# Performance work log

Hardware: AMD Instinct MI355X
Metric: run time of the kernel (lower is better)

The kernel has to match this reference:

```python
import jax, jax.numpy as jnp
import numpy as np

EPS = 1e-5
H = 1024      # hidden_size
HH = 256      # hyper_hidden_size
E = 32        # hyper_embed_size
D = 512       # input_size
B = 4096      # batch
FORGET_BIAS = 1.0


def _ln(x, w, b):
    mu = x.mean(-1, keepdims=True)
    var = x.var(-1, keepdims=True)
    return (x - mu) * jax.lax.rsqrt(var + EPS) * w + b


def _chunk_ln(x, w, b, chunks):
    # normalize each of `chunks` equal slices independently, then single affine
    bsz = x.shape[0]
    u = x.shape[1] // chunks
    xr = x.reshape(bsz, chunks, u)
    mu = xr.mean(-1, keepdims=True)
    var = xr.var(-1, keepdims=True)
    xr = (xr - mu) * jax.lax.rsqrt(var + EPS)
    return xr.reshape(bsz, chunks * u) * w + b


def _ln_lstm_step(x, h, c, w_ih, w_hh, lnh_w, lnh_b, lnc_w, lnc_b):
    # LayerNormLSTMCell (dropout = identity, eval mode)
    lin = _chunk_ln(x @ w_ih.T + h @ w_hh.T, lnh_w, lnh_b, 4)
    i_g, f_g, o_g, c_cand = jnp.split(lin, 4, axis=1)
    c = jax.nn.sigmoid(f_g + FORGET_BIAS) * c + jax.nn.sigmoid(i_g) * jnp.tanh(c_cand)
    h = jax.nn.sigmoid(o_g) * jnp.tanh(_ln(c, lnc_w, lnc_b))
    return h, c


def _forward(x, h_total, c_total,
             hyp_w_ih, hyp_w_hh, hyp_lnh_w, hyp_lnh_b, hyp_lnc_w, hyp_lnc_b,
             w_ih, w_hh, lnh_w, lnh_b, lnc_w, lnc_b,
             sx_w0, sx_b0, sx_w1, sh_w0, sh_b0, sh_w1, bh_w0, bh_w1):
    h, h_hyper = h_total[:, :H], h_total[:, H:]
    c, c_hyper = c_total[:, :H], c_total[:, H:]

    h_hyper, c_hyper = _ln_lstm_step(x, h_hyper, c_hyper, hyp_w_ih, hyp_w_hh,
                                     hyp_lnh_w, hyp_lnh_b, hyp_lnc_w, hyp_lnc_b)

    bsz = x.shape[0]
    Wx = (x @ w_ih.T).reshape(bsz, 4, H)   # [B,4,H]
    Wh = (h @ w_hh.T).reshape(bsz, 4, H)

    # hypernetwork scale/bias nets, batched over the 4 gates (g)
    scale_x = jnp.einsum('bge,goe->bgo', jnp.einsum('bi,gei->bge', h_hyper, sx_w0) + sx_b0, sx_w1)
    scale_h = jnp.einsum('bge,goe->bgo', jnp.einsum('bi,gei->bge', h_hyper, sh_w0) + sh_b0, sh_w1)
    bias_h = jnp.einsum('bge,goe->bgo', jnp.einsum('bi,gei->bge', h_hyper, bh_w0), bh_w1)

    gates = (scale_x * Wx + scale_h * Wh + bias_h).reshape(bsz, 4 * H)
    gates = _chunk_ln(gates, lnh_w, lnh_b, 4)
    i_g, f_g, o_g, c_cand = jnp.split(gates, 4, axis=1)
    c = jax.nn.sigmoid(f_g + FORGET_BIAS) * c + jax.nn.sigmoid(i_g) * jnp.tanh(c_cand)
    h = jax.nn.sigmoid(o_g) * jnp.tanh(_ln(c, lnc_w, lnc_b))

    h_total = jnp.concatenate([h, h_hyper], axis=1)
    c_total = jnp.concatenate([c, c_hyper], axis=1)
    return h, h_total, c_total


def setup_inputs() -> dict:
    key = jax.random.key(0)
    ks = jax.random.split(key, 24)
    rn = lambda k, shape, s: jax.random.normal(k, shape, dtype=jnp.float32) * s
    inp = {
        'x': rn(ks[0], (B, D), 1.0),
        'h_total': rn(ks[1], (B, H + HH), 1.0),
        'c_total': rn(ks[2], (B, H + HH), 1.0),
        # hyper cell (LayerNormLSTMCell) params
        'hyp_w_ih': rn(ks[3], (4 * HH, D), 0.05),
        'hyp_w_hh': rn(ks[4], (4 * HH, HH), 0.06),
        'hyp_lnh_w': jnp.ones((4 * HH,), jnp.float32),
        'hyp_lnh_b': jnp.zeros((4 * HH,), jnp.float32),
        'hyp_lnc_w': jnp.ones((HH,), jnp.float32),
        'hyp_lnc_b': jnp.zeros((HH,), jnp.float32),
        # main cell params
        'w_ih': rn(ks[5], (4 * H, D), 0.04),
        'w_hh': rn(ks[6], (4 * H, H), 0.03),
        'lnh_w': jnp.ones((4 * H,), jnp.float32),
        'lnh_b': jnp.zeros((4 * H,), jnp.float32),
        'lnc_w': jnp.ones((H,), jnp.float32),
        'lnc_b': jnp.zeros((H,), jnp.float32),
        # norms_x: 4 HyperNorms (scale net only): Linear(HH->E, bias) + Linear(E->H, no bias)
        'sx_w0': rn(ks[7], (4, E, HH), 0.01),
        'sx_b0': jnp.ones((4, E), jnp.float32),
        'sx_w1': rn(ks[8], (4, H, E), 0.1 / E),
        # norms_h: scale net + bias net
        'sh_w0': rn(ks[9], (4, E, HH), 0.01),
        'sh_b0': jnp.ones((4, E), jnp.float32),
        'sh_w1': rn(ks[10], (4, H, E), 0.1 / E),
        'bh_w0': rn(ks[11], (4, E, HH), 0.01),
        'bh_w1': rn(ks[12], (4, H, E), 0.01),
    }
    return inp


def reference(x, h_total, c_total,
              hyp_w_ih, hyp_w_hh, hyp_lnh_w, hyp_lnh_b, hyp_lnc_w, hyp_lnc_b,
              w_ih, w_hh, lnh_w, lnh_b, lnc_w, lnc_b,
              sx_w0, sx_b0, sx_w1, sh_w0, sh_b0, sh_w1, bh_w0, bh_w1):
    return _forward(x, h_total, c_total,
                    hyp_w_ih, hyp_w_hh, hyp_lnh_w, hyp_lnh_b, hyp_lnc_w, hyp_lnc_b,
                    w_ih, w_hh, lnh_w, lnh_b, lnc_w, lnc_b,
                    sx_w0, sx_b0, sx_w1, sh_w0, sh_b0, sh_w1, bh_w0, bh_w1)
```

## Files before the change

### kernel.cpp

```cpp
#include <hip/hip_runtime.h>
#include <math.h>

typedef unsigned short u16;
typedef unsigned int u32;
typedef unsigned long long u64;
typedef __attribute__((ext_vector_type(4))) float vf4;
typedef __attribute__((ext_vector_type(8))) _Float16 f16x8;

#define EPSV 1e-5f
#define BB 4096
#define LDT 1280

__device__ __forceinline__ float sigf(float x){
  float e = expf(-fabsf(x));
  float r = 1.f/(1.f+e);
  return x>=0.f ? r : 1.f-r;
}

__device__ __forceinline__ float wave_sum(float v){
  #pragma unroll
  for (int m=32;m>0;m>>=1) v += __shfl_xor(v, m);
  return v;
}

#define AS1 __attribute__((address_space(1)))
#define AS3 __attribute__((address_space(3)))
__device__ __forceinline__ void gload_lds16(const u16* g, u16* l){
  __builtin_amdgcn_global_load_lds((const AS1 void*)g, (AS3 void*)l, 16, 0, 0);
}

__global__ __launch_bounds__(64) void cvt_half(const float* __restrict__ in, int ld_in, int K,
                                               u16* __restrict__ out, int ld_out)
{
  int row = blockIdx.y;
  int c4 = (blockIdx.x*64 + threadIdx.x)*4;
  if (c4 >= K) return;
  float4 v = *(const float4*)(in + (size_t)row*ld_in + c4);
  float vv[4] = {v.x, v.y, v.z, v.w};
  u64 pk=0;
  #pragma unroll
  for (int j=0;j<4;j++){
    _Float16 h = (_Float16)vv[j];
    pk |= (u64)__builtin_bit_cast(u16, h) << (16*j);
  }
  *(u64*)(out + (size_t)row*ld_out + c4) = pk;
}

template<int P>
__device__ __forceinline__ void load_afrag(const u16* Ab, int wm, int lm, int kg, f16x8 af[2][2]){
  #pragma unroll
  for (int fl=0; fl<2; fl++)
    #pragma unroll
    for (int kk=0; kk<2; kk++){
      int row = wm*128 + (P*2+fl)*16 + lm;
      int sl = (kk*4+kg) ^ (row&7);
      af[fl][kk] = *(const f16x8*)(Ab + row*64 + sl*8);
    }
}

template<int P>
__device__ __forceinline__ void mfma_phase(vf4 acc[8][4], const f16x8 af[2][2], const f16x8 bf[4][2]){
  __builtin_amdgcn_s_setprio(1);
  #pragma unroll
  for (int fl=0; fl<2; fl++)
    #pragma unroll
    for (int j=0; j<4; j++)
      #pragma unroll
      for (int kk=0; kk<2; kk++)
        acc[P*2+fl][j] = __builtin_amdgcn_mfma_f32_16x16x32_f16(af[fl][kk], bf[j][kk], acc[P*2+fl][j], 0, 0, 0);
  __builtin_amdgcn_s_setprio(0);
}

__global__ __launch_bounds__(512, 2) void gemm256(
    const u16* __restrict__ A, int lda,
    const u16* __restrict__ B, int ldb,
    float* __restrict__ C, int ldc, int K)
{
  __shared__ u16 As[2][256*64];
  __shared__ u16 Bs[2][256*64];
  const int tid = threadIdx.x;
  const int lane = tid & 63;
  const int wid = tid >> 6;
  const int wm = wid >> 2, wn = wid & 3;
  const int m0 = blockIdx.y*256, n0 = blockIdx.x*256;
  const int kg = lane>>4, lm = lane&15;

  vf4 acc[8][4];
  #pragma unroll
  for (int i=0;i<8;i++)
    #pragma unroll
    for (int j=0;j<4;j++) acc[i][j] = (vf4){0.f,0.f,0.f,0.f};

  const u16* gA[4]; const u16* gB[4]; int ldsOff[4];
  #pragma unroll
  for (int q=0;q<4;q++){
    int c = q*512 + tid;
    int row = c>>3, slot = c&7;
    int scol = slot ^ (row&7);
    gA[q] = A + (size_t)(m0+row)*lda + scol*8;
    gB[q] = B + (size_t)(n0+row)*ldb + scol*8;
    ldsOff[q] = (q*512 + wid*64)*8;
  }

  const int NT = K>>6;
  #pragma unroll
  for (int q=0;q<4;q++) gload_lds16(gA[q], &As[0][ldsOff[q]]);
  #pragma unroll
  for (int q=0;q<4;q++) gload_lds16(gB[q], &Bs[0][ldsOff[q]]);
  asm volatile("s_waitcnt vmcnt(0)" ::: "memory");
  __builtin_amdgcn_s_barrier();

  f16x8 afA[2][2], afB[2][2], bfrag[4][2];

  for (int t=0; t<NT; ++t){
    const int cur = t&1, nxt = cur^1;
    const u16* Ab = As[cur];
    const u16* Bb = Bs[cur];

    load_afrag<0>(Ab, wm, lm, kg, afA);
    #pragma unroll
    for (int j=0;j<4;j++)
      #pragma unroll
      for (int kk=0;kk<2;kk++){
        int row = wn*64 + j*16 + lm;
        int sl = (kk*4+kg) ^ (row&7);
        bfrag[j][kk] = *(const f16x8*)(Bb + row*64 + sl*8);
      }
    load_afrag<1>(Ab, wm, lm, kg, afB);
    if (t+1 < NT){
      const int kb = (t+1)<<6;
      #pragma unroll
      for (int q=0;q<4;q++) gload_lds16(gA[q]+kb, &As[nxt][ldsOff[q]]);
      #pragma unroll
      for (int q=0;q<4;q++) gload_lds16(gB[q]+kb, &Bs[nxt][ldsOff[q]]);
    }
    __builtin_amdgcn_sched_barrier(0);
    __builtin_amdgcn_s_barrier();
    mfma_phase<0>(acc, afA, bfrag);
    __builtin_amdgcn_s_barrier();

    load_afrag<2>(Ab, wm, lm, kg, afA);
    __builtin_amdgcn_sched_barrier(0);
    __builtin_amdgcn_s_barrier();
    mfma_phase<1>(acc, afB, bfrag);
    __builtin_amdgcn_s_barrier();

    load_afrag<3>(Ab, wm, lm, kg, afB);
    __builtin_amdgcn_sched_barrier(0);
    __builtin_amdgcn_s_barrier();
    mfma_phase<2>(acc, afA, bfrag);
    __builtin_amdgcn_s_barrier();

    __builtin_amdgcn_sched_barrier(0);
    __builtin_amdgcn_s_barrier();
    mfma_phase<3>(acc, afB, bfrag);
    asm volatile("s_waitcnt vmcnt(0)" ::: "memory");
    __builtin_amdgcn_s_barrier();
  }

  #pragma unroll
  for (int f=0; f<8; f++){
    int rb = m0 + wm*128 + f*16 + kg*4;
    #pragma unroll
    for (int j=0; j<4; j++){
      int cc = n0 + wn*64 + j*16 + lm;
      #pragma unroll
      for (int r=0; r<4; r++)
        C[(size_t)(rb+r)*ldc + cc] = acc[f][j][r];
    }
  }
}

__global__ __launch_bounds__(256) void gemm_f16nt(
    const u16* __restrict__ A, int lda,
    const u16* __restrict__ B, int ldb,
    float* __restrict__ C, int ldc,
    int K, int accflag)
{
  __shared__ u16 As[128*32];
  __shared__ u16 Bs[128*32];
  const int tid = threadIdx.x;
  const int lane = tid & 63;
  const int w = tid >> 6;
  const int wr = w >> 1, wc = w & 1;
  const int m0 = blockIdx.y*128, n0 = blockIdx.x*128;

  vf4 acc[4][4];
  #pragma unroll
  for (int i=0;i<4;i++)
    #pragma unroll
    for (int j=0;j<4;j++) acc[i][j] = (vf4){0.f,0.f,0.f,0.f};

  const int c0i = w*128 + lane;
  const int c1i = c0i + 64;
  const int r0i = c0i>>2, s0i = (c0i&3) ^ ((r0i>>1)&3);
  const int r1i = c1i>>2, s1i = (c1i&3) ^ ((r1i>>1)&3);
  const u16* gA0 = A + (size_t)(m0+r0i)*lda + s0i*8;
  const u16* gA1 = A + (size_t)(m0+r1i)*lda + s1i*8;
  const u16* gB0 = B + (size_t)(n0+r0i)*ldb + s0i*8;
  const u16* gB1 = B + (size_t)(n0+r1i)*ldb + s1i*8;
  u16* lA0 = As + w*1024;
  u16* lA1 = As + w*1024 + 512;
  u16* lB0 = Bs + w*1024;
  u16* lB1 = Bs + w*1024 + 512;

  const int kg = lane>>4, lm = lane&15;

  for (int k0=0; k0<K; k0+=32){
    __syncthreads();
    gload_lds16(gA0 + k0, lA0);
    gload_lds16(gA1 + k0, lA1);
    gload_lds16(gB0 + k0, lB0);
    gload_lds16(gB1 + k0, lB1);
    __syncthreads();
    f16x8 af[4], bfr[4];
    #pragma unroll
    for (int i=0;i<4;i++){
      int ra = wr*64 + i*16 + lm;
      int sa = kg ^ ((ra>>1)&3);
      af[i] = *(const f16x8*)(As + ra*32 + sa*8);
      int rb = wc*64 + i*16 + lm;
      int sb = kg ^ ((rb>>1)&3);
      bfr[i] = *(const f16x8*)(Bs + rb*32 + sb*8);
    }
    #pragma unroll
    for (int i=0;i<4;i++)
      #pragma unroll
      for (int j=0;j<4;j++)
        acc[i][j] = __builtin_amdgcn_mfma_f32_16x16x32_f16(af[i], bfr[j], acc[i][j], 0, 0, 0);
  }

  const int lhi = lane>>4;
  #pragma unroll
  for (int i=0;i<4;i++){
    int rbase = m0 + wr*64 + i*16 + lhi*4;
    #pragma unroll
    for (int j=0;j<4;j++){
      int cc = n0 + wc*64 + j*16 + lm;
      #pragma unroll
      for (int r=0;r<4;r++){
        float v = acc[i][j][r];
        float* pC = C + (size_t)(rbase+r)*ldc + cc;
        if (accflag) v += *pC;
        *pC = v;
      }
    }
  }
}

__global__ __launch_bounds__(256) void hyper_cell(
    const float* __restrict__ lin, const float* __restrict__ c_in,
    const float* __restrict__ lnh_w, const float* __restrict__ lnh_b,
    const float* __restrict__ lnc_w, const float* __restrict__ lnc_b,
    float* __restrict__ ht_out, float* __restrict__ ct_out)
{
  int b=blockIdx.x, tid=threadIdx.x, lane=tid&63, w=tid>>6;
  __shared__ float ly[1024];
  __shared__ float red[4];
  float4 t = *(const float4*)(lin + (size_t)b*1024 + tid*4);
  float v[4]={t.x,t.y,t.z,t.w};
  float s = wave_sum(v[0]+v[1]+v[2]+v[3]);
  float mu = s*(1.f/256.f);
  float q=0.f;
  #pragma unroll
  for (int j=0;j<4;j++){ float d=v[j]-mu; q+=d*d; }
  q = wave_sum(q);
  float rs = rsqrtf(q*(1.f/256.f)+EPSV);
  int base = tid*4;
  #pragma unroll
  for (int j=0;j<4;j++) ly[base+j] = (v[j]-mu)*rs*lnh_w[base+j]+lnh_b[base+j];
  __syncthreads();
  float ig=ly[tid], fg=ly[256+tid], og=ly[512+tid], cc=ly[768+tid];
  float co = c_in[(size_t)b*LDT + 1024 + tid];
  float cn = sigf(fg+1.f)*co + sigf(ig)*tanhf(cc);
  float s2 = wave_sum(cn);
  if(lane==0) red[w]=s2;
  __syncthreads();
  float mu2=(red[0]+red[1]+red[2]+red[3])*(1.f/256.f);
  __syncthreads();
  float d = cn-mu2;
  float q2 = wave_sum(d*d);
  if(lane==0) red[w]=q2;
  __syncthreads();
  float rs2 = rsqrtf((red[0]+red[1]+red[2]+red[3])*(1.f/256.f)+EPSV);
  float hh = sigf(og)*tanhf(d*rs2*lnc_w[tid]+lnc_b[tid]);
  ht_out[(size_t)b*LDT+1024+tid]=hh;
  ct_out[(size_t)b*LDT+1024+tid]=cn;
}

#define EST 68
__device__ __forceinline__ void stage_dot(
    const float* __restrict__ zp, const float* __restrict__ wp, const float* __restrict__ bias,
    int r0, int gc0, int g, int tid, int tx, int ty,
    float (&acc)[4][4], float* Zs, float* Ws)
{
  const int lr = tid>>2;
  const int le4 = (tid&3)<<2;
  float4 zv0 = *(const float4*)(zp + (size_t)(r0+lr)*384 + g*32 + le4);
  float4 zv1 = *(const float4*)(zp + (size_t)(r0+lr)*384 + g*32 + le4 + 16);
  if (bias){
    zv0.x += bias[g*32+le4+0]; zv0.y += bias[g*32+le4+1];
    zv0.z += bias[g*32+le4+2]; zv0.w += bias[g*32+le4+3];
    zv1.x += bias[g*32+le4+16]; zv1.y += bias[g*32+le4+17];
    zv1.z += bias[g*32+le4+18]; zv1.w += bias[g*32+le4+19];
  }
  float4 wv0 = *(const float4*)(wp + ((size_t)(g*1024 + gc0 + lr))*32 + le4);
  float4 wv1 = *(const float4*)(wp + ((size_t)(g*1024 + gc0 + lr))*32 + le4 + 16);
  __syncthreads();
  Zs[(le4+0)*EST+lr]=zv0.x; Zs[(le4+1)*EST+lr]=zv0.y; Zs[(le4+2)*EST+lr]=zv0.z; Zs[(le4+3)*EST+lr]=zv0.w;
  Zs[(le4+16)*EST+lr]=zv1.x; Zs[(le4+17)*EST+lr]=zv1.y; Zs[(le4+18)*EST+lr]=zv1.z; Zs[(le4+19)*EST+lr]=zv1.w;
  Ws[(le4+0)*EST+lr]=wv0.x; Ws[(le4+1)*EST+lr]=wv0.y; Ws[(le4+2)*EST+lr]=wv0.z; Ws[(le4+3)*EST+lr]=wv0.w;
  Ws[(le4+16)*EST+lr]=wv1.x; Ws[(le4+17)*EST+lr]=wv1.y; Ws[(le4+18)*EST+lr]=wv1.z; Ws[(le4+19)*EST+lr]=wv1.w;
  __syncthreads();
  #pragma unroll
  for (int i=0;i<4;i++)
    #pragma unroll
    for (int j=0;j<4;j++) acc[i][j]=0.f;
  #pragma unroll
  for (int e=0;e<32;e++){
    float4 av = *(const float4*)&Zs[e*EST + ty*4];
    float4 bv = *(const float4*)&Ws[e*EST + tx*4];
    float a[4]={av.x,av.y,av.z,av.w}, b[4]={bv.x,bv.y,bv.z,bv.w};
    #pragma unroll
    for (int i=0;i<4;i++)
      #pragma unroll
      for (int j=0;j<4;j++) acc[i][j]+=a[i]*b[j];
  }
}

__global__ __launch_bounds__(256) void scale_apply(
  const float* __restrict__ Wx, const float* __restrict__ Wh,
  const float* __restrict__ zcat,
  const float* __restrict__ b0x, const float* __restrict__ b0h,
  const float* __restrict__ w1x, const float* __restrict__ w1h, const float* __restrict__ w1b,
  float* __restrict__ glin)
{
  __shared__ float Zs[32*EST], Ws[32*EST];
  int tid=threadIdx.x;
  int c0=blockIdx.x*64, r0=blockIdx.y*64;
  int g=c0>>10, gc0=c0&1023;
  int tx=tid&15, ty=tid>>4;
  float acc[4][4], gval[4][4];

  stage_dot(zcat,     w1x, b0x, r0, gc0, g, tid, tx, ty, acc, Zs, Ws);
  #pragma unroll
  for (int i=0;i<4;i++){
    float4 wv = *(const float4*)(Wx + (size_t)(r0+ty*4+i)*4096 + c0 + tx*4);
    gval[i][0]=acc[i][0]*wv.x; gval[i][1]=acc[i][1]*wv.y;
    gval[i][2]=acc[i][2]*wv.z; gval[i][3]=acc[i][3]*wv.w;
  }
  stage_dot(zcat+128, w1h, b0h, r0, gc0, g, tid, tx, ty, acc, Zs, Ws);
  #pragma unroll
  for (int i=0;i<4;i++){
    float4 wv = *(const float4*)(Wh + (size_t)(r0+ty*4+i)*4096 + c0 + tx*4);
    gval[i][0]+=acc[i][0]*wv.x; gval[i][1]+=acc[i][1]*wv.y;
    gval[i][2]+=acc[i][2]*wv.z; gval[i][3]+=acc[i][3]*wv.w;
  }
  stage_dot(zcat+256, w1b, nullptr, r0, gc0, g, tid, tx, ty, acc, Zs, Ws);
  #pragma unroll
  for (int i=0;i<4;i++){
    float4 v;
    v.x=gval[i][0]+acc[i][0]; v.y=gval[i][1]+acc[i][1];
    v.z=gval[i][2]+acc[i][2]; v.w=gval[i][3]+acc[i][3];
    *(float4*)(glin + (size_t)(r0+ty*4+i)*4096 + c0 + tx*4) = v;
  }
}

__global__ __launch_bounds__(256) void main_cell(
    const float* __restrict__ glin, const float* __restrict__ c_in,
    const float* __restrict__ lnh_w, const float* __restrict__ lnh_b,
    const float* __restrict__ lnc_w, const float* __restrict__ lnc_b,
    float* __restrict__ h_out, float* __restrict__ ht_out, float* __restrict__ ct_out)
{
  int b=blockIdx.x, tid=threadIdx.x, lane=tid&63, w=tid>>6;
  __shared__ float red[16];
  float v[4][4];
  #pragma unroll
  for (int g=0;g<4;g++){
    float4 t = *(const float4*)(glin + (size_t)b*4096 + g*1024 + tid*4);
    v[g][0]=t.x; v[g][1]=t.y; v[g][2]=t.z; v[g][3]=t.w;
  }
  float mu[4], rs[4];
  #pragma unroll
  for (int g=0;g<4;g++){
    float s = wave_sum(v[g][0]+v[g][1]+v[g][2]+v[g][3]);
    if(lane==0) red[g*4+w]=s;
  }
  __syncthreads();
  #pragma unroll
  for (int g=0;g<4;g++) mu[g]=(red[g*4]+red[g*4+1]+red[g*4+2]+red[g*4+3])*(1.f/1024.f);
  __syncthreads();
  #pragma unroll
  for (int g=0;g<4;g++){
    float q=0.f;
    #pragma unroll
    for (int j=0;j<4;j++){ float d=v[g][j]-mu[g]; q+=d*d; }
    q = wave_sum(q);
    if(lane==0) red[g*4+w]=q;
  }
  __syncthreads();
  #pragma unroll
  for (int g=0;g<4;g++) rs[g]=rsqrtf((red[g*4]+red[g*4+1]+red[g*4+2]+red[g*4+3])*(1.f/1024.f)+EPSV);
  int o0=tid*4;
  float y[4][4];
  #pragma unroll
  for (int g=0;g<4;g++)
    #pragma unroll
    for (int j=0;j<4;j++){
      int idx=g*1024+o0+j;
      y[g][j]=(v[g][j]-mu[g])*rs[g]*lnh_w[idx]+lnh_b[idx];
    }
  float4 ct = *(const float4*)(c_in + (size_t)b*LDT + o0);
  float co[4]={ct.x,ct.y,ct.z,ct.w};
  float cn[4];
  #pragma unroll
  for (int j=0;j<4;j++) cn[j]=sigf(y[1][j]+1.f)*co[j] + sigf(y[0][j])*tanhf(y[3][j]);
  float s = wave_sum(cn[0]+cn[1]+cn[2]+cn[3]);
  __syncthreads();
  if(lane==0) red[w]=s;
  __syncthreads();
  float muc=(red[0]+red[1]+red[2]+red[3])*(1.f/1024.f);
  __syncthreads();
  float q=0.f;
  #pragma unroll
  for (int j=0;j<4;j++){ float d=cn[j]-muc; q+=d*d; }
  q=wave_sum(q);
  if(lane==0) red[w]=q;
  __syncthreads();
  float rsc=rsqrtf((red[0]+red[1]+red[2]+red[3])*(1.f/1024.f)+EPSV);
  float h[4];
  #pragma unroll
  for (int j=0;j<4;j++) h[j]=sigf(y[2][j])*tanhf((cn[j]-muc)*rsc*lnc_w[o0+j]+lnc_b[o0+j]);
  float4 hv; hv.x=h[0]; hv.y=h[1]; hv.z=h[2]; hv.w=h[3];
  float4 cv; cv.x=cn[0]; cv.y=cn[1]; cv.z=cn[2]; cv.w=cn[3];
  *(float4*)(h_out +(size_t)b*1024+o0) = hv;
  *(float4*)(ht_out+(size_t)b*LDT +o0) = hv;
  *(float4*)(ct_out+(size_t)b*LDT +o0) = cv;
}

extern "C" void kernel_launch(void* const* d_in, const int* in_sizes, int n_in,
                              void* d_out, int out_size, void* d_ws, size_t ws_size,
                              hipStream_t stream) {
  (void)in_sizes; (void)n_in; (void)out_size; (void)ws_size;
  const float* x         = (const float*)d_in[0];
  const float* h_total   = (const float*)d_in[1];
  const float* c_total   = (const float*)d_in[2];
  const float* hyp_w_ih  = (const float*)d_in[3];
  const float* hyp_w_hh  = (const float*)d_in[4];
  const float* hyp_lnh_w = (const float*)d_in[5];
  const float* hyp_lnh_b = (const float*)d_in[6];
  const float* hyp_lnc_w = (const float*)d_in[7];
  const float* hyp_lnc_b = (const float*)d_in[8];
  const float* w_ih      = (const float*)d_in[9];
  const float* w_hh      = (const float*)d_in[10];
  const float* lnh_w     = (const float*)d_in[11];
  const float* lnh_b     = (const float*)d_in[12];
  const float* lnc_w     = (const float*)d_in[13];
  const float* lnc_b     = (const float*)d_in[14];
  const float* sx_w0     = (const float*)d_in[15];
  const float* sx_b0     = (const float*)d_in[16];
  const float* sx_w1     = (const float*)d_in[17];
  const float* sh_w0     = (const float*)d_in[18];
  const float* sh_b0     = (const float*)d_in[19];
  const float* sh_w1     = (const float*)d_in[20];
  const float* bh_w0     = (const float*)d_in[21];
  const float* bh_w1     = (const float*)d_in[22];

  float* out    = (float*)d_out;
  float* h_out  = out;
  float* ht_out = out + (size_t)BB*1024;
  float* ct_out = ht_out + (size_t)BB*LDT;

  char* p = (char*)d_ws;
  float* lin   = (float*)p; p += (size_t)4096*1024*4;
  float* Wx    = (float*)p; p += (size_t)4096*4096*4;
  float* Wh    = (float*)p; p += (size_t)4096*4096*4;
  float* zcat  = (float*)p; p += (size_t)4096*384*4;
  u16* Hbig    = (u16*)p;   p += (size_t)4096*1024*2;
  u16* Wihb    = (u16*)p;   p += (size_t)4096*512*2;
  u16* Whhb    = (u16*)p;   p += (size_t)4096*1024*2;
  u16* XHhyp   = (u16*)p;   p += (size_t)4096*768*2;
  u16* Whyp    = (u16*)p;   p += (size_t)1024*768*2;
  u16* Hhyp16  = (u16*)p;   p += (size_t)4096*256*2;
  u16* Zw      = (u16*)p;   p += (size_t)384*256*2;

  cvt_half<<<dim3(2,4096),64,0,stream>>>(x, 512, 512, XHhyp, 768);
  cvt_half<<<dim3(1,4096),64,0,stream>>>(h_total+1024, LDT, 256, XHhyp+512, 768);
  cvt_half<<<dim3(4,4096),64,0,stream>>>(h_total, LDT, 1024, Hbig, 1024);
  cvt_half<<<dim3(2,4096),64,0,stream>>>(w_ih, 512, 512, Wihb, 512);
  cvt_half<<<dim3(4,4096),64,0,stream>>>(w_hh, 1024, 1024, Whhb, 1024);
  cvt_half<<<dim3(2,1024),64,0,stream>>>(hyp_w_ih, 512, 512, Whyp, 768);
  cvt_half<<<dim3(1,1024),64,0,stream>>>(hyp_w_hh, 256, 256, Whyp+512, 768);
  cvt_half<<<dim3(1,128),64,0,stream>>>(sx_w0, 256, 256, Zw, 256);
  cvt_half<<<dim3(1,128),64,0,stream>>>(sh_w0, 256, 256, Zw+(size_t)128*256, 256);
  cvt_half<<<dim3(1,128),64,0,stream>>>(bh_w0, 256, 256, Zw+(size_t)256*256, 256);

  gemm_f16nt<<<dim3(8,32),256,0,stream>>>(XHhyp,768, Whyp,768, lin,1024, 768, 0);
  gemm256<<<dim3(16,16),512,0,stream>>>(XHhyp,768, Wihb,512, Wx,4096, 512);
  gemm256<<<dim3(16,16),512,0,stream>>>(Hbig,1024, Whhb,1024, Wh,4096, 1024);

  hyper_cell<<<4096,256,0,stream>>>(lin, c_total, hyp_lnh_w, hyp_lnh_b, hyp_lnc_w, hyp_lnc_b, ht_out, ct_out);

  cvt_half<<<dim3(1,4096),64,0,stream>>>(ht_out+1024, LDT, 256, Hhyp16, 256);
  gemm_f16nt<<<dim3(3,32),256,0,stream>>>(Hhyp16,256, Zw,256, zcat,384, 256, 0);

  scale_apply<<<dim3(64,64),256,0,stream>>>(Wx, Wh, zcat, sx_b0, sh_b0, sx_w1, sh_w1, bh_w1, Wx);
  main_cell<<<4096,256,0,stream>>>(Wx, c_total, lnh_w, lnh_b, lnc_w, lnc_b, h_out, ht_out, ct_out);
}
```

Before: 427.4 us.

## Use MFMA for hypernet scale stage, merge conversions, fuse hhyp fp16 output

Replaces the fp32 LDS-tiled scale_apply with an MFMA-based kernel that loads fp16 z and w1 fragments directly and applies the Wx/Wh scaling in registers. The ten cvt_half launches become five merged conversion kernels. hyper_cell now writes the fp16 hyper hidden state itself, which removes a separate conversion pass. A dedicated gemm_zout adds the biases and writes z in fp16. The aim is to cut FP32 FMA work and launch overhead. In exchange, z and w1 lose precision, and the Wx/Wh reads in the MFMA output layout are only partly coalesced.

```diff
diff --git a/kernel.cpp b/kernel.cpp
--- a/kernel.cpp
+++ b/kernel.cpp
@@ -29,21 +29,76 @@
   __builtin_amdgcn_global_load_lds((const AS1 void*)g, (AS3 void*)l, 16, 0, 0);
 }
 
-__global__ __launch_bounds__(64) void cvt_half(const float* __restrict__ in, int ld_in, int K,
-                                               u16* __restrict__ out, int ld_out)
-{
-  int row = blockIdx.y;
-  int c4 = (blockIdx.x*64 + threadIdx.x)*4;
-  if (c4 >= K) return;
-  float4 v = *(const float4*)(in + (size_t)row*ld_in + c4);
+__device__ __forceinline__ u64 pack_half4(float4 v){
+  u64 pk=0;
   float vv[4] = {v.x, v.y, v.z, v.w};
-  u64 pk=0;
   #pragma unroll
   for (int j=0;j<4;j++){
     _Float16 h = (_Float16)vv[j];
     pk |= (u64)__builtin_bit_cast(u16, h) << (16*j);
   }
-  *(u64*)(out + (size_t)row*ld_out + c4) = pk;
+  return pk;
+}
+
+__global__ __launch_bounds__(64) void cvt_acts(const float* __restrict__ x,
+                                               const float* __restrict__ h_total,
+                                               u16* __restrict__ XHhyp, u16* __restrict__ Hbig)
+{
+  int row = blockIdx.y;
+  int c4 = (blockIdx.x*64 + threadIdx.x)*4;
+  if (c4 >= 1792) return;
+  const float* src; u16* dst;
+  if (c4 < 512){ src = x + (size_t)row*512 + c4;                 dst = XHhyp + (size_t)row*768 + c4; }
+  else if (c4 < 1536){ src = h_total + (size_t)row*LDT + (c4-512); dst = Hbig + (size_t)row*1024 + (c4-512); }
+  else { src = h_total + (size_t)row*LDT + 1024 + (c4-1536);     dst = XHhyp + (size_t)row*768 + 512 + (c4-1536); }
+  *(u64*)dst = pack_half4(*(const float4*)src);
+}
+
+__global__ __launch_bounds__(64) void cvt_wmain(const float* __restrict__ w_ih,
+                                                const float* __restrict__ w_hh,
+                                                u16* __restrict__ Wihb, u16* __restrict__ Whhb)
+{
+  int row = blockIdx.y;
+  int c4 = (blockIdx.x*64 + threadIdx.x)*4;
+  if (c4 >= 1536) return;
+  const float* src; u16* dst;
+  if (c4 < 512){ src = w_ih + (size_t)row*512 + c4;  dst = Wihb + (size_t)row*512 + c4; }
+  else { src = w_hh + (size_t)row*1024 + (c4-512);   dst = Whhb + (size_t)row*1024 + (c4-512); }
+  *(u64*)dst = pack_half4(*(const float4*)src);
+}
+
+__global__ __launch_bounds__(64) void cvt_whyp(const float* __restrict__ wih,
+                                               const float* __restrict__ whh,
+                                               u16* __restrict__ Whyp)
+{
+  int row = blockIdx.y;
+  int c4 = (blockIdx.x*64 + threadIdx.x)*4;
+  if (c4 >= 768) return;
+  const float* src = (c4 < 512) ? (wih + (size_t)row*512 + c4) : (whh + (size_t)row*256 + (c4-512));
+  *(u64*)(Whyp + (size_t)row*768 + c4) = pack_half4(*(const float4*)src);
+}
+
+__global__ __launch_bounds__(64) void cvt_zw(const float* __restrict__ w0x,
+                                             const float* __restrict__ w0h,
+                                             const float* __restrict__ w0b,
+                                             u16* __restrict__ Zw)
+{
+  int row = blockIdx.y;
+  int c4 = threadIdx.x*4;
+  const float* src = (row<128) ? (w0x + (size_t)row*256) : (row<256 ? (w0h + (size_t)(row-128)*256) : (w0b + (size_t)(row-256)*256));
+  *(u64*)(Zw + (size_t)row*256 + c4) = pack_half4(*(const float4*)(src + c4));
+}
+
+__global__ __launch_bounds__(256) void cvt_w1(const float* __restrict__ w1x,
+                                              const float* __restrict__ w1h,
+                                              const float* __restrict__ w1b,
+                                              u16* __restrict__ w1cat16)
+{
+  int i4 = (blockIdx.x*256 + threadIdx.x)*4;
+  int t = i4 >> 17;
+  int off = i4 & 131071;
+  const float* src = (t==0) ? w1x : (t==1 ? w1h : w1b);
+  *(u64*)(w1cat16 + i4) = pack_half4(*(const float4*)(src + off));
 }
 
 template<int P>
@@ -248,11 +303,88 @@
   }
 }
 
+__global__ __launch_bounds__(256) void gemm_zout(
+    const u16* __restrict__ A,
+    const u16* __restrict__ B,
+    const float* __restrict__ b0x, const float* __restrict__ b0h,
+    u16* __restrict__ Cz)
+{
+  __shared__ u16 As[128*32];
+  __shared__ u16 Bs[128*32];
+  const int tid = threadIdx.x;
+  const int lane = tid & 63;
+  const int w = tid >> 6;
+  const int wr = w >> 1, wc = w & 1;
+  const int m0 = blockIdx.y*128, n0 = blockIdx.x*128;
+
+  vf4 acc[4][4];
+  #pragma unroll
+  for (int i=0;i<4;i++)
+    #pragma unroll
+    for (int j=0;j<4;j++) acc[i][j] = (vf4){0.f,0.f,0.f,0.f};
+
+  const int c0i = w*128 + lane;
+  const int c1i = c0i + 64;
+  const int r0i = c0i>>2, s0i = (c0i&3) ^ ((r0i>>1)&3);
+  const int r1i = c1i>>2, s1i = (c1i&3) ^ ((r1i>>1)&3);
+  const u16* gA0 = A + (size_t)(m0+r0i)*256 + s0i*8;
+  const u16* gA1 = A + (size_t)(m0+r1i)*256 + s1i*8;
+  const u16* gB0 = B + (size_t)(n0+r0i)*256 + s0i*8;
+  const u16* gB1 = B + (size_t)(n0+r1i)*256 + s1i*8;
+  u16* lA0 = As + w*1024;
+  u16* lA1 = As + w*1024 + 512;
+  u16* lB0 = Bs + w*1024;
+  u16* lB1 = Bs + w*1024 + 512;
+
+  const int kg = lane>>4, lm = lane&15;
+
+  for (int k0=0; k0<256; k0+=32){
+    __syncthreads();
+    gload_lds16(gA0 + k0, lA0);
+    gload_lds16(gA1 + k0, lA1);
+    gload_lds16(gB0 + k0, lB0);
+    gload_lds16(gB1 + k0, lB1);
+    __syncthreads();
+    f16x8 af[4], bfr[4];
+    #pragma unroll
+    for (int i=0;i<4;i++){
+      int ra = wr*64 + i*16 + lm;
+      int sa = kg ^ ((ra>>1)&3);
+      af[i] = *(const f16x8*)(As + ra*32 + sa*8);
+      int rb = wc*64 + i*16 + lm;
+      int sb = kg ^ ((rb>>1)&3);
+      bfr[i] = *(const f16x8*)(Bs + rb*32 + sb*8);
+    }
+    #pragma unroll
+    for (int i=0;i<4;i++)
+      #pragma unroll
+      for (int j=0;j<4;j++)
+        acc[i][j] = __builtin_amdgcn_mfma_f32_16x16x32_f16(af[i], bfr[j], acc[i][j], 0, 0, 0);
+  }
+
+  const int lhi = lane>>4;
+  #pragma unroll
+  for (int i=0;i<4;i++){
+    int rbase = m0 + wr*64 + i*16 + lhi*4;
+    #pragma unroll
+    for (int j=0;j<4;j++){
+      int cc = n0 + wc*64 + j*16 + lm;
+      float bias = (cc<128) ? b0x[cc] : (cc<256 ? b0h[cc-128] : 0.f);
+      #pragma unroll
+      for (int r=0;r<4;r++){
+        _Float16 h = (_Float16)(acc[i][j][r] + bias);
+        Cz[(size_t)(rbase+r)*384 + cc] = __builtin_bit_cast(u16, h);
+      }
+    }
+  }
+}
+
 __global__ __launch_bounds__(256) void hyper_cell(
     const float* __restrict__ lin, const float* __restrict__ c_in,
     const float* __restrict__ lnh_w, const float* __restrict__ lnh_b,
     const float* __restrict__ lnc_w, const float* __restrict__ lnc_b,
-    float* __restrict__ ht_out, float* __restrict__ ct_out)
+    float* __restrict__ ht_out, float* __restrict__ ct_out,
+    u16* __restrict__ hhyp16)
 {
   int b=blockIdx.x, tid=threadIdx.x, lane=tid&63, w=tid>>6;
   __shared__ float ly[1024];
@@ -286,83 +418,115 @@
   float hh = sigf(og)*tanhf(d*rs2*lnc_w[tid]+lnc_b[tid]);
   ht_out[(size_t)b*LDT+1024+tid]=hh;
   ct_out[(size_t)b*LDT+1024+tid]=cn;
-}
-
-#define EST 68
-__device__ __forceinline__ void stage_dot(
-    const float* __restrict__ zp, const float* __restrict__ wp, const float* __restrict__ bias,
-    int r0, int gc0, int g, int tid, int tx, int ty,
-    float (&acc)[4][4], float* Zs, float* Ws)
-{
-  const int lr = tid>>2;
-  const int le4 = (tid&3)<<2;
-  float4 zv0 = *(const float4*)(zp + (size_t)(r0+lr)*384 + g*32 + le4);
-  float4 zv1 = *(const float4*)(zp + (size_t)(r0+lr)*384 + g*32 + le4 + 16);
-  if (bias){
-    zv0.x += bias[g*32+le4+0]; zv0.y += bias[g*32+le4+1];
-    zv0.z += bias[g*32+le4+2]; zv0.w += bias[g*32+le4+3];
-    zv1.x += bias[g*32+le4+16]; zv1.y += bias[g*32+le4+17];
-    zv1.z += bias[g*32+le4+18]; zv1.w += bias[g*32+le4+19];
-  }
-  float4 wv0 = *(const float4*)(wp + ((size_t)(g*1024 + gc0 + lr))*32 + le4);
-  float4 wv1 = *(const float4*)(wp + ((size_t)(g*1024 + gc0 + lr))*32 + le4 + 16);
-  __syncthreads();
-  Zs[(le4+0)*EST+lr]=zv0.x; Zs[(le4+1)*EST+lr]=zv0.y; Zs[(le4+2)*EST+lr]=zv0.z; Zs[(le4+3)*EST+lr]=zv0.w;
-  Zs[(le4+16)*EST+lr]=zv1.x; Zs[(le4+17)*EST+lr]=zv1.y; Zs[(le4+18)*EST+lr]=zv1.z; Zs[(le4+19)*EST+lr]=zv1.w;
-  Ws[(le4+0)*EST+lr]=wv0.x; Ws[(le4+1)*EST+lr]=wv0.y; Ws[(le4+2)*EST+lr]=wv0.z; Ws[(le4+3)*EST+lr]=wv0.w;
-  Ws[(le4+16)*EST+lr]=wv1.x; Ws[(le4+17)*EST+lr]=wv1.y; Ws[(le4+18)*EST+lr]=wv1.z; Ws[(le4+19)*EST+lr]=wv1.w;
-  __syncthreads();
+  _Float16 h16 = (_Float16)hh;
+  hhyp16[(size_t)b*256+tid] = __builtin_bit_cast(u16, h16);
+}
+
+__global__ __launch_bounds__(256) void scale_mfma(
+    const u16* __restrict__ zcat16,
+    const u16* __restrict__ w1cat16,
+    const float* __restrict__ Wx, const float* __restrict__ Wh,
+    float* __restrict__ glin)
+{
+  const int tid = threadIdx.x;
+  const int lane = tid & 63;
+  const int w = tid >> 6;
+  const int wr = w >> 1, wc = w & 1;
+  const int m0 = blockIdx.y*128;
+  const int n0 = blockIdx.x*128;
+  const int g = n0 >> 10, gc = n0 & 1023;
+  const int kg = lane>>4, lm = lane&15;
+
+  vf4 gval[4][4];
+  vf4 sacc[4][4];
+  f16x8 af[4], bf[4];
+
+  #pragma unroll
+  for (int i=0;i<4;i++){
+    int row = m0 + wr*64 + i*16 + lm;
+    af[i] = *(const f16x8*)(zcat16 + (size_t)row*384 + 0*128 + g*32 + kg*8);
+  }
+  #pragma unroll
+  for (int j=0;j<4;j++){
+    int col = gc + wc*64 + j*16 + lm;
+    bf[j] = *(const f16x8*)(w1cat16 + 0*131072 + (size_t)(g*1024 + col)*32 + kg*8);
+  }
   #pragma unroll
   for (int i=0;i<4;i++)
     #pragma unroll
-    for (int j=0;j<4;j++) acc[i][j]=0.f;
-  #pragma unroll
-  for (int e=0;e<32;e++){
-    float4 av = *(const float4*)&Zs[e*EST + ty*4];
-    float4 bv = *(const float4*)&Ws[e*EST + tx*4];
-    float a[4]={av.x,av.y,av.z,av.w}, b[4]={bv.x,bv.y,bv.z,bv.w};
-    #pragma unroll
-    for (int i=0;i<4;i++)
-      #pragma unroll
-      for (int j=0;j<4;j++) acc[i][j]+=a[i]*b[j];
-  }
-}
-
-__global__ __launch_bounds__(256) void scale_apply(
-  const float* __restrict__ Wx, const float* __restrict__ Wh,
-  const float* __restrict__ zcat,
-  const float* __restrict__ b0x, const float* __restrict__ b0h,
-  const float* __restrict__ w1x, const float* __restrict__ w1h, const float* __restrict__ w1b,
-  float* __restrict__ glin)
-{
-  __shared__ float Zs[32*EST], Ws[32*EST];
-  int tid=threadIdx.x;
-  int c0=blockIdx.x*64, r0=blockIdx.y*64;
-  int g=c0>>10, gc0=c0&1023;
-  int tx=tid&15, ty=tid>>4;
-  float acc[4][4], gval[4][4];
-
-  stage_dot(zcat,     w1x, b0x, r0, gc0, g, tid, tx, ty, acc, Zs, Ws);
-  #pragma unroll
-  for (int i=0;i<4;i++){
-    float4 wv = *(const float4*)(Wx + (size_t)(r0+ty*4+i)*4096 + c0 + tx*4);
-    gval[i][0]=acc[i][0]*wv.x; gval[i][1]=acc[i][1]*wv.y;
-    gval[i][2]=acc[i][2]*wv.z; gval[i][3]=acc[i][3]*wv.w;
-  }
-  stage_dot(zcat+128, w1h, b0h, r0, gc0, g, tid, tx, ty, acc, Zs, Ws);
-  #pragma unroll
-  for (int i=0;i<4;i++){
-    float4 wv = *(const float4*)(Wh + (size_t)(r0+ty*4+i)*4096 + c0 + tx*4);
-    gval[i][0]+=acc[i][0]*wv.x; gval[i][1]+=acc[i][1]*wv.y;
-    gval[i][2]+=acc[i][2]*wv.z; gval[i][3]+=acc[i][3]*wv.w;
-  }
-  stage_dot(zcat+256, w1b, nullptr, r0, gc0, g, tid, tx, ty, acc, Zs, Ws);
-  #pragma unroll
-  for (int i=0;i<4;i++){
-    float4 v;
-    v.x=gval[i][0]+acc[i][0]; v.y=gval[i][1]+acc[i][1];
-    v.z=gval[i][2]+acc[i][2]; v.w=gval[i][3]+acc[i][3];
-    *(float4*)(glin + (size_t)(r0+ty*4+i)*4096 + c0 + tx*4) = v;
+    for (int j=0;j<4;j++){
+      sacc[i][j] = (vf4){0.f,0.f,0.f,0.f};
+      sacc[i][j] = __builtin_amdgcn_mfma_f32_16x16x32_f16(af[i], bf[j], sacc[i][j], 0, 0, 0);
+    }
+  #pragma unroll
+  for (int i=0;i<4;i++){
+    int rb = m0 + wr*64 + i*16 + kg*4;
+    #pragma unroll
+    for (int j=0;j<4;j++){
+      int cc = n0 + wc*64 + j*16 + lm;
+      #pragma unroll
+      for (int r=0;r<4;r++)
+        gval[i][j][r] = sacc[i][j][r] * Wx[(size_t)(rb+r)*4096 + cc];
+    }
+  }
+
+  #pragma unroll
+  for (int i=0;i<4;i++){
+    int row = m0 + wr*64 + i*16 + lm;
+    af[i] = *(const f16x8*)(zcat16 + (size_t)row*384 + 1*128 + g*32 + kg*8);
+  }
+  #pragma unroll
+  for (int j=0;j<4;j++){
+    int col = gc + wc*64 + j*16 + lm;
+    bf[j] = *(const f16x8*)(w1cat16 + 1*131072 + (size_t)(g*1024 + col)*32 + kg*8);
+  }
+  #pragma unroll
+  for (int i=0;i<4;i++)
+    #pragma unroll
+    for (int j=0;j<4;j++){
+      sacc[i][j] = (vf4){0.f,0.f,0.f,0.f};
+      sacc[i][j] = __builtin_amdgcn_mfma_f32_16x16x32_f16(af[i], bf[j], sacc[i][j], 0, 0, 0);
+    }
+  #pragma unroll
+  for (int i=0;i<4;i++){
+    int rb = m0 + wr*64 + i*16 + kg*4;
+    #pragma unroll
+    for (int j=0;j<4;j++){
+      int cc = n0 + wc*64 + j*16 + lm;
+      #pragma unroll
+      for (int r=0;r<4;r++)
+        gval[i][j][r] += sacc[i][j][r] * Wh[(size_t)(rb+r)*4096 + cc];
+    }
+  }
+
+  #pragma unroll
+  for (int i=0;i<4;i++){
+    int row = m0 + wr*64 + i*16 + lm;
+    af[i] = *(const f16x8*)(zcat16 + (size_t)row*384 + 2*128 + g*32 + kg*8);
+  }
+  #pragma unroll
+  for (int j=0;j<4;j++){
+    int col = gc + wc*64 + j*16 + lm;
+    bf[j] = *(const f16x8*)(w1cat16 + 2*131072 + (size_t)(g*1024 + col)*32 + kg*8);
+  }
+  #pragma unroll
+  for (int i=0;i<4;i++)
+    #pragma unroll
+    for (int j=0;j<4;j++){
+      sacc[i][j] = (vf4){0.f,0.f,0.f,0.f};
+      sacc[i][j] = __builtin_amdgcn_mfma_f32_16x16x32_f16(af[i], bf[j], sacc[i][j], 0, 0, 0);
+    }
+
+  #pragma unroll
+  for (int i=0;i<4;i++){
+    int rb = m0 + wr*64 + i*16 + kg*4;
+    #pragma unroll
+    for (int j=0;j<4;j++){
+      int cc = n0 + wc*64 + j*16 + lm;
+      #pragma unroll
+      for (int r=0;r<4;r++)
+        glin[(size_t)(rb+r)*4096 + cc] = gval[i][j][r] + sacc[i][j][r];
+    }
   }
 }
 
@@ -472,38 +636,35 @@
   float* ct_out = ht_out + (size_t)BB*LDT;
 
   char* p = (char*)d_ws;
-  float* lin   = (float*)p; p += (size_t)4096*1024*4;
-  float* Wx    = (float*)p; p += (size_t)4096*4096*4;
-  float* Wh    = (float*)p; p += (size_t)4096*4096*4;
-  float* zcat  = (float*)p; p += (size_t)4096*384*4;
-  u16* Hbig    = (u16*)p;   p += (size_t)4096*1024*2;
-  u16* Wihb    = (u16*)p;   p += (size_t)4096*512*2;
-  u16* Whhb    = (u16*)p;   p += (size_t)4096*1024*2;
-  u16* XHhyp   = (u16*)p;   p += (size_t)4096*768*2;
-  u16* Whyp    = (u16*)p;   p += (size_t)1024*768*2;
-  u16* Hhyp16  = (u16*)p;   p += (size_t)4096*256*2;
-  u16* Zw      = (u16*)p;   p += (size_t)384*256*2;
-
-  cvt_half<<<dim3(2,4096),64,0,stream>>>(x, 512, 512, XHhyp, 768);
-  cvt_half<<<dim3(1,4096),64,0,stream>>>(h_total+1024, LDT, 256, XHhyp+512, 768);
-  cvt_half<<<dim3(4,4096),64,0,stream>>>(h_total, LDT, 1024, Hbig, 1024);
-  cvt_half<<<dim3(2,4096),64,0,stream>>>(w_ih, 512, 512, Wihb, 512);
-  cvt_half<<<dim3(4,4096),64,0,stream>>>(w_hh, 1024, 1024, Whhb, 1024);
-  cvt_half<<<dim3(2,1024),64,0,stream>>>(hyp_w_ih, 512, 512, Whyp, 768);
-  cvt_half<<<dim3(1,1024),64,0,stream>>>(hyp_w_hh, 256, 256, Whyp+512, 768);
-  cvt_half<<<dim3(1,128),64,0,stream>>>(sx_w0, 256, 256, Zw, 256);
-  cvt_half<<<dim3(1,128),64,0,stream>>>(sh_w0, 256, 256, Zw+(size_t)128*256, 256);
-  cvt_half<<<dim3(1,128),64,0,stream>>>(bh_w0, 256, 256, Zw+(size_t)256*256, 256);
+  float* lin    = (float*)p; p += (size_t)4096*1024*4;
+  float* Wx     = (float*)p; p += (size_t)4096*4096*4;
+  float* Wh     = (float*)p; p += (size_t)4096*4096*4;
+  u16* Hbig     = (u16*)p;   p += (size_t)4096*1024*2;
+  u16* Wihb     = (u16*)p;   p += (size_t)4096*512*2;
+  u16* Whhb     = (u16*)p;   p += (size_t)4096*1024*2;
+  u16* XHhyp    = (u16*)p;   p += (size_t)4096*768*2;
+  u16* Whyp     = (u16*)p;   p += (size_t)1024*768*2;
+  u16* Hhyp16   = (u16*)p;   p += (size_t)4096*256*2;
+  u16* Zw       = (u16*)p;   p += (size_t)384*256*2;
+  u16* zcat16   = (u16*)p;   p += (size_t)4096*384*2;
+  u16* w1cat16  = (u16*)p;   p += (size_t)3*131072*2;
+
+  cvt_acts <<<dim3(7,4096),64,0,stream>>>(x, h_total, XHhyp, Hbig);
+  cvt_wmain<<<dim3(6,4096),64,0,stream>>>(w_ih, w_hh, Wihb, Whhb);
+  cvt_whyp <<<dim3(3,1024),64,0,stream>>>(hyp_w_ih, hyp_w_hh, Whyp);
+  cvt_zw   <<<dim3(1,384),64,0,stream>>>(sx_w0, sh_w0, bh_w0, Zw);
+  cvt_w1   <<<384,256,0,stream>>>(sx_w1, sh_w1, bh_w1, w1cat16);
 
   gemm_f16nt<<<dim3(8,32),256,0,stream>>>(XHhyp,768, Whyp,768, lin,1024, 768, 0);
   gemm256<<<dim3(16,16),512,0,stream>>>(XHhyp,768, Wihb,512, Wx,4096, 512);
   gemm256<<<dim3(16,16),512,0,stream>>>(Hbig,1024, Whhb,1024, Wh,4096, 1024);
 
-  hyper_cell<<<4096,256,0,stream>>>(lin, c_total, hyp_lnh_w, hyp_lnh_b, hyp_lnc_w, hyp_lnc_b, ht_out, ct_out);
-
-  cvt_half<<<dim3(1,4096),64,0,stream>>>(ht_out+1024, LDT, 256, Hhyp16, 256);
-  gemm_f16nt<<<dim3(3,32),256,0,stream>>>(Hhyp16,256, Zw,256, zcat,384, 256, 0);
-
-  scale_apply<<<dim3(64,64),256,0,stream>>>(Wx, Wh, zcat, sx_b0, sh_b0, sx_w1, sh_w1, bh_w1, Wx);
+  hyper_cell<<<4096,256,0,stream>>>(lin, c_total, hyp_lnh_w, hyp_lnh_b, hyp_lnc_w, hyp_lnc_b,
+                                    ht_out, ct_out, Hhyp16);
+
+  gemm_zout<<<dim3(3,32),256,0,stream>>>(Hhyp16, Zw, sx_b0, sh_b0, zcat16);
+
+  scale_mfma<<<dim3(32,32),256,0,stream>>>(zcat16, w1cat16, Wx, Wh, Wx);
+
   main_cell<<<4096,256,0,stream>>>(Wx, c_total, lnh_w, lnh_b, lnc_w, lnc_b, h_out, ht_out, ct_out);
 }
```

After: 352.7 us. -17.5%, faster.
